# Performance work log

Measured on AMD Instinct MI355X. Metric: run time of the kernel, lower is better.

Reference implementation:

```python
import jax, jax.numpy as jnp
import numpy as np
import itertools

B, RES, RES_, STRIDE = 256, 14, 7, 2
N, N_ = RES * RES, RES_ * RES_
IN_DIM, OUT_DIM = 384, 512
H, KD, AR = 12, 32, 2
D = AR * KD            # 64, per-head value dim
DH = D * H             # 768
NH_KD = KD * H         # 384
KV_H = DH + NH_KD      # 1152
EPS = 1e-5


def _bias_idxs():
    # Replicates the relative-offset indexing from __init__.
    points = list(itertools.product(range(RES), range(RES)))
    points_ = list(itertools.product(range(RES_), range(RES_)))
    offsets, idxs = {}, []
    for p1 in points_:
        for p2 in points:
            off = (abs(p1[0] * STRIDE - p2[0]), abs(p1[1] * STRIDE - p2[1]))
            if off not in offsets:
                offsets[off] = len(offsets)
            idxs.append(offsets[off])
    return np.array(idxs, dtype=np.int32).reshape(N_, N), len(offsets)


def linear_bn(x, w, gamma, beta, mean, var):
    # Linear (no bias) followed by BatchNorm1d in inference form (fused affine).
    s = gamma / jnp.sqrt(var + EPS)
    return jnp.matmul(x, w.T) * s + (beta - mean * s)


def setup_inputs() -> dict:
    key = jax.random.key(0)
    ks = jax.random.split(key, 12)
    idxs_np, n_off = _bias_idxs()

    def bn_params(k, dim):
        k1, k2, k3, k4 = jax.random.split(k, 4)
        return (jax.random.normal(k1, (dim,)) * 0.1 + 1.0,   # gamma
                jax.random.normal(k2, (dim,)) * 0.1,          # beta
                jax.random.normal(k3, (dim,)) * 0.1,          # running_mean
                jax.random.uniform(k4, (dim,), minval=0.5, maxval=1.5))  # running_var

    kv_g, kv_b, kv_m, kv_v = bn_params(ks[1], KV_H)
    q_g, q_b, q_m, q_v = bn_params(ks[3], NH_KD)
    pr_g, pr_b, pr_m, pr_v = bn_params(ks[5], OUT_DIM)

    return {
        "x": jax.random.normal(ks[0], (B, N, IN_DIM), dtype=jnp.float32),
        "kv_w": jax.random.normal(ks[6], (KV_H, IN_DIM), dtype=jnp.float32) * (IN_DIM ** -0.5),
        "kv_g": kv_g, "kv_b": kv_b, "kv_m": kv_m, "kv_v": kv_v,
        "q_w": jax.random.normal(ks[7], (NH_KD, IN_DIM), dtype=jnp.float32) * (IN_DIM ** -0.5),
        "q_g": q_g, "q_b": q_b, "q_m": q_m, "q_v": q_v,
        "proj_w": jax.random.normal(ks[8], (OUT_DIM, DH), dtype=jnp.float32) * (DH ** -0.5),
        "proj_g": pr_g, "proj_b": pr_b, "proj_m": pr_m, "proj_v": pr_v,
        "attention_biases": jax.random.normal(ks[9], (H, n_off), dtype=jnp.float32) * 0.02,
        "bias_idxs": jnp.asarray(idxs_np),
    }


def reference(x, kv_w, kv_g, kv_b, kv_m, kv_v,
              q_w, q_g, q_b, q_m, q_v,
              proj_w, proj_g, proj_b, proj_m, proj_v,
              attention_biases, bias_idxs):
    Bsz = x.shape[0]
    scale = KD ** -0.5
    # kv projection: [B, N, H, KD+D] -> split into k, v
    kv = linear_bn(x, kv_w, kv_g, kv_b, kv_m, kv_v).reshape(Bsz, N, H, KD + D)
    k, v = kv[..., :KD], kv[..., KD:]
    # strided subsample of queries: [B, 14, 14, C] -> [B, 49, C]
    xs = x.reshape(Bsz, RES, RES, IN_DIM)[:, ::STRIDE, ::STRIDE].reshape(Bsz, N_, IN_DIM)
    q = linear_bn(xs, q_w, q_g, q_b, q_m, q_v).reshape(Bsz, N_, H, KD)
    # attention with gathered relative-position bias: bias [H, N_, N]
    bias = attention_biases[:, bias_idxs]
    attn = jnp.einsum('bqhd,bkhd->bhqk', q, k) * scale + bias
    attn = jax.nn.softmax(attn, axis=-1)
    out = jnp.einsum('bhqk,bkhd->bqhd', attn, v).reshape(Bsz, N_, DH)
    out = jax.nn.hard_swish(out)
    return linear_bn(out, proj_w, proj_g, proj_b, proj_m, proj_v)
```

## Files before the change

### kernel.cpp

```cpp
#include <hip/hip_runtime.h>
#include <hip/hip_bf16.h>
#include <math.h>

typedef unsigned short U16;
typedef unsigned int U32;
typedef __attribute__((ext_vector_type(8))) short bf8;
typedef __attribute__((ext_vector_type(4))) float f4;
typedef __attribute__((ext_vector_type(4))) unsigned short u16x4;

#define AS1 __attribute__((address_space(1)))
#define AS3 __attribute__((address_space(3)))

#define BSZ   256
#define NTOK  196
#define NQ    49
#define INDIM 384
#define OUTD  512
#define NH    12
#define DV    64
#define DHD   768
#define KVH   1152
#define NPADR 224

__device__ inline U16 f2bf(float f){
    __hip_bfloat16 h = __float2bfloat16(f);
    return *(U16*)&h;
}
__device__ inline f4 f4zero(){ f4 z; z[0]=0.f; z[1]=0.f; z[2]=0.f; z[3]=0.f; return z; }
__device__ inline bf8 bf8zero(){ bf8 v;
#pragma unroll
    for (int j=0;j<8;++j) v[j]=0; return v; }

#define XC_N   (BSZ*NTOK*INDIM/8)
#define XC_BLK (XC_N/256)
#define W1C (KVH*INDIM/8)
#define W2C (INDIM*INDIM/8)
#define W3C (OUTD*DHD/8)
#define WC_N   (W1C+W2C+W3C)
#define WC_BLK (WC_N/256)
#define BIAS_N   (NH*NQ*NTOK)
#define BIAS_BLK ((BIAS_N+255)/256)
#define BN_BLK   ((KVH+INDIM+OUTD)/256)
__global__ void k_prep(const float* __restrict__ x, U16* __restrict__ x_bf,
                       const float* __restrict__ w1, const float* __restrict__ w2,
                       const float* __restrict__ w3, U16* __restrict__ o1,
                       U16* __restrict__ o2, U16* __restrict__ o3,
                       const float* __restrict__ ab, const int* __restrict__ idxs, int n_off,
                       const float* __restrict__ g1, const float* __restrict__ b1,
                       const float* __restrict__ m1, const float* __restrict__ v1,
                       const float* __restrict__ g2, const float* __restrict__ b2,
                       const float* __restrict__ m2, const float* __restrict__ v2,
                       const float* __restrict__ g3, const float* __restrict__ b3,
                       const float* __restrict__ m3, const float* __restrict__ v3,
                       float* __restrict__ s1, float* __restrict__ bo1,
                       float* __restrict__ s2, float* __restrict__ bo2,
                       float* __restrict__ s3, float* __restrict__ bo3,
                       float* __restrict__ bias_out){
    const int blk = blockIdx.x;
    const int tid = threadIdx.x;
    if (blk < XC_BLK){
        int i = blk*256 + tid;
        const float* p = x + (size_t)i*8;
        U16 o[8];
#pragma unroll
        for (int j=0;j<8;++j) o[j] = f2bf(p[j]);
        *(bf8*)(x_bf + (size_t)i*8) = *(const bf8*)o;
    } else if (blk < XC_BLK + WC_BLK){
        int i = (blk-XC_BLK)*256 + tid;
        const float* p; U16* o;
        if (i < W1C){ p = w1 + (size_t)i*8; o = o1 + (size_t)i*8; }
        else if (i < W1C+W2C){ int k=i-W1C; p = w2 + (size_t)k*8; o = o2 + (size_t)k*8; }
        else { int k=i-W1C-W2C; p = w3 + (size_t)k*8; o = o3 + (size_t)k*8; }
        U16 t[8];
#pragma unroll
        for (int j=0;j<8;++j) t[j] = f2bf(p[j]);
        *(bf8*)o = *(const bf8*)t;
    } else if (blk < XC_BLK + WC_BLK + BIAS_BLK){
        int i = (blk-XC_BLK-WC_BLK)*256 + tid;
        if (i < BIAS_N){
            int h = i / (NQ*NTOK);
            int qk = i - h*(NQ*NTOK);
            bias_out[i] = ab[h*n_off + idxs[qk]];
        }
    } else {
        int i = (blk-XC_BLK-WC_BLK-BIAS_BLK)*256 + tid;
        const float *g,*b,*m,*v; float *so,*bo; int k;
        if (i < KVH){ g=g1;b=b1;m=m1;v=v1;so=s1;bo=bo1;k=i; }
        else if (i < KVH+INDIM){ g=g2;b=b2;m=m2;v=v2;so=s2;bo=bo2;k=i-KVH; }
        else { g=g3;b=b3;m=m3;v=v3;so=s3;bo=bo3;k=i-KVH-INDIM; }
        float s = g[k] / sqrtf(v[k] + 1e-5f);
        so[k] = s;
        bo[k] = b[k] - m[k]*s;
    }
}

#define KLO 12800
__global__ __launch_bounds__(256,2) void k_fused(
    const U16* __restrict__ xbf, const U16* __restrict__ kvw, const U16* __restrict__ qo_,
    const float* __restrict__ skv, const float* __restrict__ bkv,
    const float* __restrict__ biasf, U16* __restrict__ aout)
{
    __shared__ U16 smem[20480];
    const int hw = blockIdx.x;
    const int bh = (hw & 7)*384 + (hw >> 3);
    const int b = bh / NH, h = bh - b*NH;
    const int tid = threadIdx.x, lane = tid & 63, w = tid >> 6;
    const int wm = w & 1, wn = w >> 1;
    const int l15 = lane & 15, oct = lane >> 4;

    U16* Ab[2] = { smem + 0,     smem + 7168 };
    U16* Bb[2] = { smem + 14336, smem + 17408 };

    U32 aoff[4];
#pragma unroll
    for (int c=0;c<3;++c){
        int s = c*256 + tid;
        int ach = s / NPADR, ar = s - ach*NPADR;
        int row = (ar < NTOK) ? ar : (NTOK-1);
        aoff[c] = (U32)(b*NTOK + row)*INDIM + ach*8;
    }
    {
        int s = 768 + (tid & 127);
        int ach = s / NPADR, ar = s - ach*NPADR;
        int row = (ar < NTOK) ? ar : (NTOK-1);
        aoff[3] = (U32)(b*NTOK + row)*INDIM + ach*8;
    }
    U32 boff[2];
    {
        int s0 = tid;
        int bc0 = s0 / 96, br0 = s0 - bc0*96;
        boff[0] = (U32)(h*96 + br0)*INDIM + bc0*8;
        int s1 = 128 + (tid | 128);
        int bc1 = s1 / 96, br1 = s1 - bc1*96;
        boff[1] = (U32)(h*96 + br1)*INDIM + bc1*8;
    }

    f4 acc[7][3];
#pragma unroll
    for (int i=0;i<7;++i)
#pragma unroll
        for (int j=0;j<3;++j) acc[i][j] = f4zero();

#define STAGE(buf, kb) do{ \
    _Pragma("unroll") \
    for (int c=0;c<3;++c) \
        __builtin_amdgcn_global_load_lds((const AS1 U32*)(xbf + aoff[c] + (kb)), \
            (AS3 U32*)(Ab[buf] + (c*256+tid)*8), 16, 0, 0); \
    if (tid < 128) \
        __builtin_amdgcn_global_load_lds((const AS1 U32*)(xbf + aoff[3] + (kb)), \
            (AS3 U32*)(Ab[buf] + (768+tid)*8), 16, 0, 0); \
    __builtin_amdgcn_global_load_lds((const AS1 U32*)(kvw + boff[0] + (kb)), \
        (AS3 U32*)(Bb[buf] + tid*8), 16, 0, 0); \
    if (tid >= 128) \
        __builtin_amdgcn_global_load_lds((const AS1 U32*)(kvw + boff[1] + (kb)), \
            (AS3 U32*)(Bb[buf] + (128+tid)*8), 16, 0, 0); \
}while(0)

    STAGE(0, 0);
    asm volatile("s_waitcnt vmcnt(0)" ::: "memory");
    __builtin_amdgcn_sched_barrier(0);
    __builtin_amdgcn_s_barrier();
    __builtin_amdgcn_sched_barrier(0);

#pragma unroll
    for (int kt=0; kt<12; ++kt){
        const int cur = kt & 1;
        if (kt < 11) STAGE(cur^1, (kt+1)*32);
        __builtin_amdgcn_sched_barrier(0);
        bf8 af[7], bfr[3];
#pragma unroll
        for (int i=0;i<7;++i)
            af[i]  = *(const bf8*)(Ab[cur] + (oct*NPADR + wm*112 + i*16 + l15)*8);
#pragma unroll
        for (int j=0;j<3;++j)
            bfr[j] = *(const bf8*)(Bb[cur] + (oct*96 + wn*48 + j*16 + l15)*8);
        __builtin_amdgcn_s_setprio(1);
#pragma unroll
        for (int i=0;i<7;++i)
#pragma unroll
            for (int j=0;j<3;++j)
                acc[i][j] = __builtin_amdgcn_mfma_f32_16x16x32_bf16(af[i], bfr[j], acc[i][j], 0, 0, 0);
        __builtin_amdgcn_s_setprio(0);
        __builtin_amdgcn_sched_barrier(0);
        asm volatile("s_waitcnt vmcnt(0)" ::: "memory");
        __builtin_amdgcn_s_barrier();
        __builtin_amdgcn_sched_barrier(0);
    }
#undef STAGE

#pragma unroll
    for (int j=0;j<3;++j){
        const int cc = wn*48 + j*16 + l15;
        const float sc = skv[h*96 + cc];
        const float bi = bkv[h*96 + cc];
#pragma unroll
        for (int i=0;i<7;++i){
            const int n0 = wm*112 + i*16 + oct*4;
            if (cc < 32){
#pragma unroll
                for (int r=0;r<4;++r)
                    smem[KLO + ((cc>>3)*NPADR + n0 + r)*8 + (cc&7)] = f2bf(acc[i][j][r]*sc + bi);
            } else if (n0 < 200){
                const int dv = cc - 32;
                u16x4 pk;
#pragma unroll
                for (int r=0;r<4;++r) pk[r] = f2bf(acc[i][j][r]*sc + bi);
                *(u16x4*)(smem + ((n0>>3)*64 + dv)*8 + (oct&1)*4) = pk;
            }
        }
    }
    __syncthreads();

    const int qg = w*16 + l15;
    bf8 qf = bf8zero();
    if (qg < NQ) qf = *(const bf8*)(qo_ + ((size_t)(b*NQ + qg))*INDIM + h*32 + oct*8);

    f4 sacc[14];
#pragma unroll
    for (int mt=0;mt<14;++mt) sacc[mt] = f4zero();
#pragma unroll
    for (int mt=0;mt<14;++mt){
        const bf8 kf = *(const bf8*)(smem + KLO + (oct*NPADR + mt*16 + l15)*8);
        sacc[mt] = __builtin_amdgcn_mfma_f32_16x16x32_bf16(kf, qf, sacc[mt], 0, 0, 0);
    }

    const float scale = 0.17677669529663689f;
    float mx = -1e30f;
#pragma unroll
    for (int mt=0;mt<14;++mt){
        const int n0 = mt*16 + oct*4;
        f4 bi4 = f4zero();
        if (qg < NQ && n0 < NTOK) bi4 = *(const f4*)(biasf + ((size_t)h*NQ + qg)*NTOK + n0);
#pragma unroll
        for (int r=0;r<4;++r){
            float s = (n0 + r < NTOK) ? sacc[mt][r]*scale + bi4[r] : -1e30f;
            sacc[mt][r] = s;
            mx = fmaxf(mx, s);
        }
    }
    mx = fmaxf(mx, __shfl_xor(mx, 16));
    mx = fmaxf(mx, __shfl_xor(mx, 32));

    float sum = 0.f;
#pragma unroll
    for (int mt=0;mt<14;++mt){
#pragma unroll
        for (int r=0;r<4;++r){
            float p = (mt*16 + oct*4 + r < NTOK) ? __expf(sacc[mt][r] - mx) : 0.f;
            sacc[mt][r] = p;
            sum += p;
        }
    }
    sum += __shfl_xor(sum, 16);
    sum += __shfl_xor(sum, 32);
    const float inv = 1.f / sum;

    const int src1 = l15 + (oct & 1)*32;
    const int src2 = src1 + 16;
    const bool hiT = (oct >> 1) != 0;
    f4 pacc[4];
#pragma unroll
    for (int dt=0;dt<4;++dt) pacc[dt] = f4zero();
#pragma unroll
    for (int kt=0;kt<7;++kt){
        const int m0 = 2*kt, m1 = 2*kt+1;
        U32 q00 = (U32)f2bf(sacc[m0][0]*inv) | ((U32)f2bf(sacc[m0][1]*inv) << 16);
        U32 q01 = (U32)f2bf(sacc[m0][2]*inv) | ((U32)f2bf(sacc[m0][3]*inv) << 16);
        U32 q10 = (U32)f2bf(sacc[m1][0]*inv) | ((U32)f2bf(sacc[m1][1]*inv) << 16);
        U32 q11 = (U32)f2bf(sacc[m1][2]*inv) | ((U32)f2bf(sacc[m1][3]*inv) << 16);
        U32 a0 = __shfl(q00, src1), a1 = __shfl(q01, src1);
        U32 c0 = __shfl(q10, src1), c1 = __shfl(q11, src1);
        U32 b0 = __shfl(q00, src2), b1 = __shfl(q01, src2);
        U32 d0 = __shfl(q10, src2), d1 = __shfl(q11, src2);
        union { U32 u[4]; bf8 v; } pu;
        pu.u[0] = hiT ? c0 : a0;
        pu.u[1] = hiT ? c1 : a1;
        pu.u[2] = hiT ? d0 : b0;
        pu.u[3] = hiT ? d1 : b1;
#pragma unroll
        for (int dt=0;dt<4;++dt){
            const bf8 vf = *(const bf8*)(smem + ((kt*4 + oct)*64 + dt*16 + l15)*8);
            pacc[dt] = __builtin_amdgcn_mfma_f32_16x16x32_bf16(pu.v, vf, pacc[dt], 0, 0, 0);
        }
    }

#pragma unroll
    for (int dt=0;dt<4;++dt){
#pragma unroll
        for (int r=0;r<4;++r){
            const int qo2 = w*16 + oct*4 + r;
            if (qo2 < NQ){
                const int d = dt*16 + l15;
                float v = pacc[dt][r];
                float tt = fminf(fmaxf(v + 3.f, 0.f), 6.f);
                aout[((size_t)(b*NQ + qo2))*DHD + h*DV + d] = f2bf(v * tt * (1.f/6.f));
            }
        }
    }
}

template<int EPI, int NK, int KD, int NTILN, int NWG, bool SUB>
__global__ __launch_bounds__(256,2) void k_g64(
    const U16* __restrict__ A, const U16* __restrict__ Bw,
    const float* __restrict__ s_arr, const float* __restrict__ b_arr,
    U16* __restrict__ o16, float* __restrict__ o32)
{
    __shared__ U16 smem[24576];
    U16* Ab[2] = { smem,          smem + 8192 };
    U16* Bb[2] = { smem + 16384,  smem + 20480 };
    constexpr int QQ = NWG/8, RR = NWG%8;
    const int xcd = blockIdx.x & 7, rest = blockIdx.x >> 3;
    const int l = (xcd < RR ? xcd*(QQ+1) : RR*(QQ+1) + (xcd-RR)*QQ) + rest;
    const int mtl = l / NTILN, ntl = l - mtl*NTILN;
    const int gm0 = mtl*128, gn0 = ntl*64;
    const int tid  = threadIdx.x;
    const int lane = tid & 63;
    const int w    = tid >> 6;
    const int wm   = w & 1, wn = w >> 1;
    const int l15  = lane & 15, oct = lane >> 4;

    f4 acc[4][2];
#pragma unroll
    for (int i=0;i<4;++i)
#pragma unroll
        for (int j=0;j<2;++j) acc[i][j] = f4zero();

    U32 aoff[4], boff[2];
#pragma unroll
    for (int c=0;c<4;++c){
        int slot = c*256 + tid;
        int row = slot & 127, ch = slot >> 7;
        int grow = gm0 + row;
        if (SUB){
            int b2 = grow / NQ, qq = grow - b2*NQ;
            grow = b2*NTOK + 28*(qq/7) + 2*(qq%7);
        }
        aoff[c] = (U32)grow*KD + ch*8;
    }
#pragma unroll
    for (int c=0;c<2;++c){
        int slot = c*256 + tid;
        int row = slot & 63, ch = slot >> 6;
        boff[c] = (U32)(gn0 + row)*KD + ch*8;
    }

#define STG(buf, kb) do{ \
    _Pragma("unroll") \
    for (int c=0;c<4;++c) \
        __builtin_amdgcn_global_load_lds((const AS1 U32*)(A + aoff[c] + (kb)), \
            (AS3 U32*)(Ab[buf] + (c*256+tid)*8), 16, 0, 0); \
    _Pragma("unroll") \
    for (int c=0;c<2;++c) \
        __builtin_amdgcn_global_load_lds((const AS1 U32*)(Bw + boff[c] + (kb)), \
            (AS3 U32*)(Bb[buf] + (c*256+tid)*8), 16, 0, 0); \
}while(0)

    STG(0, 0);

#pragma unroll
    for (int kt=0; kt<NK; ++kt){
        const int cur = kt & 1;
        if (kt+1 < NK){
            STG(cur^1, (kt+1)*64);
            asm volatile("s_waitcnt vmcnt(6)" ::: "memory");
        } else {
            asm volatile("s_waitcnt vmcnt(0)" ::: "memory");
        }
        __builtin_amdgcn_sched_barrier(0);
        __builtin_amdgcn_s_barrier();
        __builtin_amdgcn_sched_barrier(0);

#pragma unroll
        for (int kk=0;kk<2;++kk){
            bf8 af[4], bfr[2];
#pragma unroll
            for (int i=0;i<4;++i)
                af[i]  = *(const bf8*)(Ab[cur] + ((kk*4+oct)*128 + wm*64 + i*16 + l15)*8);
#pragma unroll
            for (int j=0;j<2;++j)
                bfr[j] = *(const bf8*)(Bb[cur] + ((kk*4+oct)*64 + wn*32 + j*16 + l15)*8);
            __builtin_amdgcn_s_setprio(1);
#pragma unroll
            for (int i=0;i<4;++i)
#pragma unroll
                for (int j=0;j<2;++j)
                    acc[i][j] = __builtin_amdgcn_mfma_f32_16x16x32_bf16(af[i], bfr[j], acc[i][j], 0, 0, 0);
            __builtin_amdgcn_s_setprio(0);
        }
        __builtin_amdgcn_sched_barrier(0);
        __builtin_amdgcn_s_barrier();
        __builtin_amdgcn_sched_barrier(0);
    }
#undef STG

#pragma unroll
    for (int j=0;j<2;++j){
        const int col = gn0 + wn*32 + j*16 + l15;
        const float sc = s_arr[col];
        const float bi = b_arr[col];
#pragma unroll
        for (int i=0;i<4;++i){
            const int row0 = gm0 + wm*64 + i*16 + oct*4;
#pragma unroll
            for (int r=0;r<4;++r){
                const float val = acc[i][j][r]*sc + bi;
                if (EPI == 0) o16[(size_t)(row0+r)*INDIM + col] = f2bf(val);
                else          o32[(size_t)(row0+r)*OUTD  + col] = val;
            }
        }
    }
}

extern "C" void kernel_launch(void* const* d_in, const int* in_sizes, int n_in,
                              void* d_out, int out_size, void* d_ws, size_t ws_size,
                              hipStream_t stream)
{
    const float* x    = (const float*)d_in[0];
    const float* kv_w = (const float*)d_in[1];
    const float* kv_g = (const float*)d_in[2];
    const float* kv_b = (const float*)d_in[3];
    const float* kv_m = (const float*)d_in[4];
    const float* kv_v = (const float*)d_in[5];
    const float* q_w  = (const float*)d_in[6];
    const float* q_g  = (const float*)d_in[7];
    const float* q_b  = (const float*)d_in[8];
    const float* q_m  = (const float*)d_in[9];
    const float* q_v  = (const float*)d_in[10];
    const float* pr_w = (const float*)d_in[11];
    const float* pr_g = (const float*)d_in[12];
    const float* pr_b = (const float*)d_in[13];
    const float* pr_m = (const float*)d_in[14];
    const float* pr_v = (const float*)d_in[15];
    const float* ab   = (const float*)d_in[16];
    const int*  idxs  = (const int*)d_in[17];
    const int n_off = in_sizes[16] / NH;

    char* ws = (char*)d_ws;
    size_t off = 0;
    auto alloc = [&](size_t bytes)->char*{
        char* p = ws + off; off += (bytes + 255) & ~(size_t)255; return p;
    };
    U16*   x_bf   = (U16*)  alloc((size_t)BSZ*NTOK*INDIM*2);
    U16*   kvw_bf = (U16*)  alloc((size_t)KVH*INDIM*2);
    U16*   qw_bf  = (U16*)  alloc((size_t)INDIM*INDIM*2);
    U16*   prw_bf = (U16*)  alloc((size_t)OUTD*DHD*2);
    float* s_kv   = (float*)alloc(KVH*4);
    float* b_kv   = (float*)alloc(KVH*4);
    float* s_q    = (float*)alloc(INDIM*4);
    float* b_q    = (float*)alloc(INDIM*4);
    float* s_pr   = (float*)alloc(OUTD*4);
    float* b_pr   = (float*)alloc(OUTD*4);
    float* biasf  = (float*)alloc(((size_t)NH*NQ*NTOK + 256)*4);
    U16*   q_out  = (U16*)  alloc((size_t)BSZ*NQ*INDIM*2);
    U16*   a_out  = (U16*)  alloc((size_t)BSZ*NQ*DHD*2);
    if (off > ws_size) return;

    k_prep<<<XC_BLK + WC_BLK + BIAS_BLK + BN_BLK, 256, 0, stream>>>(
        x, x_bf, kv_w, q_w, pr_w, kvw_bf, qw_bf, prw_bf,
        ab, idxs, n_off,
        kv_g, kv_b, kv_m, kv_v, q_g, q_b, q_m, q_v, pr_g, pr_b, pr_m, pr_v,
        s_kv, b_kv, s_q, b_q, s_pr, b_pr, biasf);

    k_g64<0, 6, INDIM, 6, 588, true><<<588, 256, 0, stream>>>(
        x_bf, qw_bf, s_q, b_q, q_out, nullptr);
    k_fused<<<BSZ*NH, 256, 0, stream>>>(x_bf, kvw_bf, q_out, s_kv, b_kv, biasf, a_out);
    k_g64<1, 12, DHD, 8, 784, false><<<784, 256, 0, stream>>>(
        a_out, prw_bf, s_pr, b_pr, nullptr, (float*)d_out);
}
```

Before: 180.0 us.

## Fuse query projection into fused attention kernel by widening KV GEMM tile

Drops the separate Q-projection GEMM launch. The fused per-(batch,head) kernel now also multiplies x by the 32 query-weight rows for its head, widening the B tile from 96 to 128 columns. Only the even-row/even-column tokens are kept and written to shared memory as Q. This removes one kernel launch and the q_out round trip through global memory. In exchange every block computes Q for all 196 tokens rather than 49, about 33% more MFMA work in the projection loop, and shared memory use per block grows.

```diff
diff --git a/kernel.cpp b/kernel.cpp
--- a/kernel.cpp
+++ b/kernel.cpp
@@ -27,9 +27,6 @@
     return *(U16*)&h;
 }
 __device__ inline f4 f4zero(){ f4 z; z[0]=0.f; z[1]=0.f; z[2]=0.f; z[3]=0.f; return z; }
-__device__ inline bf8 bf8zero(){ bf8 v;
-#pragma unroll
-    for (int j=0;j<8;++j) v[j]=0; return v; }
 
 #define XC_N   (BSZ*NTOK*INDIM/8)
 #define XC_BLK (XC_N/256)
@@ -95,12 +92,14 @@
 }
 
 #define KLO 12800
+#define QLO 19968
 __global__ __launch_bounds__(256,2) void k_fused(
-    const U16* __restrict__ xbf, const U16* __restrict__ kvw, const U16* __restrict__ qo_,
+    const U16* __restrict__ xbf, const U16* __restrict__ kvw, const U16* __restrict__ qw,
     const float* __restrict__ skv, const float* __restrict__ bkv,
+    const float* __restrict__ sq,  const float* __restrict__ bq,
     const float* __restrict__ biasf, U16* __restrict__ aout)
 {
-    __shared__ U16 smem[20480];
+    __shared__ U16 smem[22528];
     const int hw = blockIdx.x;
     const int bh = (hw & 7)*384 + (hw >> 3);
     const int b = bh / NH, h = bh - b*NH;
@@ -109,7 +108,7 @@
     const int l15 = lane & 15, oct = lane >> 4;
 
     U16* Ab[2] = { smem + 0,     smem + 7168 };
-    U16* Bb[2] = { smem + 14336, smem + 17408 };
+    U16* Bb[2] = { smem + 14336, smem + 18432 };
 
     U32 aoff[4];
 #pragma unroll
@@ -125,21 +124,20 @@
         int row = (ar < NTOK) ? ar : (NTOK-1);
         aoff[3] = (U32)(b*NTOK + row)*INDIM + ach*8;
     }
-    U32 boff[2];
-    {
-        int s0 = tid;
-        int bc0 = s0 / 96, br0 = s0 - bc0*96;
-        boff[0] = (U32)(h*96 + br0)*INDIM + bc0*8;
-        int s1 = 128 + (tid | 128);
-        int bc1 = s1 / 96, br1 = s1 - bc1*96;
-        boff[1] = (U32)(h*96 + br1)*INDIM + bc1*8;
-    }
-
-    f4 acc[7][3];
+    const U16* bbase[2];
+#pragma unroll
+    for (int c=0;c<2;++c){
+        int s = c*256 + tid;
+        int bc = s >> 7, br = s & 127;
+        bbase[c] = (br < 96) ? kvw + ((size_t)(h*96 + br))*INDIM + bc*8
+                             : qw  + ((size_t)(h*32 + (br-96)))*INDIM + bc*8;
+    }
+
+    f4 acc[7][4];
 #pragma unroll
     for (int i=0;i<7;++i)
 #pragma unroll
-        for (int j=0;j<3;++j) acc[i][j] = f4zero();
+        for (int j=0;j<4;++j) acc[i][j] = f4zero();
 
 #define STAGE(buf, kb) do{ \
     _Pragma("unroll") \
@@ -149,11 +147,10 @@
     if (tid < 128) \
         __builtin_amdgcn_global_load_lds((const AS1 U32*)(xbf + aoff[3] + (kb)), \
             (AS3 U32*)(Ab[buf] + (768+tid)*8), 16, 0, 0); \
-    __builtin_amdgcn_global_load_lds((const AS1 U32*)(kvw + boff[0] + (kb)), \
-        (AS3 U32*)(Bb[buf] + tid*8), 16, 0, 0); \
-    if (tid >= 128) \
-        __builtin_amdgcn_global_load_lds((const AS1 U32*)(kvw + boff[1] + (kb)), \
-            (AS3 U32*)(Bb[buf] + (128+tid)*8), 16, 0, 0); \
+    _Pragma("unroll") \
+    for (int c=0;c<2;++c) \
+        __builtin_amdgcn_global_load_lds((const AS1 U32*)(bbase[c] + (kb)), \
+            (AS3 U32*)(Bb[buf] + (c*256+tid)*8), 16, 0, 0); \
 }while(0)
 
     STAGE(0, 0);
@@ -167,18 +164,18 @@
         const int cur = kt & 1;
         if (kt < 11) STAGE(cur^1, (kt+1)*32);
         __builtin_amdgcn_sched_barrier(0);
-        bf8 af[7], bfr[3];
+        bf8 af[7], bfr[4];
 #pragma unroll
         for (int i=0;i<7;++i)
             af[i]  = *(const bf8*)(Ab[cur] + (oct*NPADR + wm*112 + i*16 + l15)*8);
 #pragma unroll
-        for (int j=0;j<3;++j)
-            bfr[j] = *(const bf8*)(Bb[cur] + (oct*96 + wn*48 + j*16 + l15)*8);
+        for (int j=0;j<4;++j)
+            bfr[j] = *(const bf8*)(Bb[cur] + (oct*128 + wn*64 + j*16 + l15)*8);
         __builtin_amdgcn_s_setprio(1);
 #pragma unroll
         for (int i=0;i<7;++i)
 #pragma unroll
-            for (int j=0;j<3;++j)
+            for (int j=0;j<4;++j)
                 acc[i][j] = __builtin_amdgcn_mfma_f32_16x16x32_bf16(af[i], bfr[j], acc[i][j], 0, 0, 0);
         __builtin_amdgcn_s_setprio(0);
         __builtin_amdgcn_sched_barrier(0);
@@ -189,10 +186,11 @@
 #undef STAGE
 
 #pragma unroll
-    for (int j=0;j<3;++j){
-        const int cc = wn*48 + j*16 + l15;
-        const float sc = skv[h*96 + cc];
-        const float bi = bkv[h*96 + cc];
+    for (int j=0;j<4;++j){
+        const int cc = wn*64 + j*16 + l15;
+        float sc, bi;
+        if (cc < 96){ sc = skv[h*96 + cc]; bi = bkv[h*96 + cc]; }
+        else        { sc = sq[h*32 + (cc-96)]; bi = bq[h*32 + (cc-96)]; }
 #pragma unroll
         for (int i=0;i<7;++i){
             const int n0 = wm*112 + i*16 + oct*4;
@@ -200,20 +198,34 @@
 #pragma unroll
                 for (int r=0;r<4;++r)
                     smem[KLO + ((cc>>3)*NPADR + n0 + r)*8 + (cc&7)] = f2bf(acc[i][j][r]*sc + bi);
-            } else if (n0 < 200){
-                const int dv = cc - 32;
-                u16x4 pk;
-#pragma unroll
-                for (int r=0;r<4;++r) pk[r] = f2bf(acc[i][j][r]*sc + bi);
-                *(u16x4*)(smem + ((n0>>3)*64 + dv)*8 + (oct&1)*4) = pk;
+            } else if (cc < 96){
+                if (n0 < 200){
+                    const int dv = cc - 32;
+                    u16x4 pk;
+#pragma unroll
+                    for (int r=0;r<4;++r) pk[r] = f2bf(acc[i][j][r]*sc + bi);
+                    *(u16x4*)(smem + ((n0>>3)*64 + dv)*8 + (oct&1)*4) = pk;
+                }
+            } else {
+                const int dq = cc - 96;
+#pragma unroll
+                for (int r=0;r<4;++r){
+                    const int n = n0 + r;
+                    if (n < NTOK && (n & 1) == 0){
+                        const int dn = n / 28, nm = n - dn*28;
+                        if (nm < 14){
+                            const int qg2 = dn*7 + (nm >> 1);
+                            smem[QLO + ((dq>>3)*64 + qg2)*8 + (dq&7)] = f2bf(acc[i][j][r]*sc + bi);
+                        }
+                    }
+                }
             }
         }
     }
     __syncthreads();
 
     const int qg = w*16 + l15;
-    bf8 qf = bf8zero();
-    if (qg < NQ) qf = *(const bf8*)(qo_ + ((size_t)(b*NQ + qg))*INDIM + h*32 + oct*8);
+    const bf8 qf = *(const bf8*)(smem + QLO + (oct*64 + qg)*8);
 
     f4 sacc[14];
 #pragma unroll
@@ -299,19 +311,18 @@
     }
 }
 
-template<int EPI, int NK, int KD, int NTILN, int NWG, bool SUB>
-__global__ __launch_bounds__(256,2) void k_g64(
+__global__ __launch_bounds__(256,2) void k_proj(
     const U16* __restrict__ A, const U16* __restrict__ Bw,
     const float* __restrict__ s_arr, const float* __restrict__ b_arr,
-    U16* __restrict__ o16, float* __restrict__ o32)
+    float* __restrict__ o32)
 {
     __shared__ U16 smem[24576];
     U16* Ab[2] = { smem,          smem + 8192 };
     U16* Bb[2] = { smem + 16384,  smem + 20480 };
-    constexpr int QQ = NWG/8, RR = NWG%8;
+    constexpr int NWG = 784, QQ = NWG/8, RR = NWG%8;
     const int xcd = blockIdx.x & 7, rest = blockIdx.x >> 3;
     const int l = (xcd < RR ? xcd*(QQ+1) : RR*(QQ+1) + (xcd-RR)*QQ) + rest;
-    const int mtl = l / NTILN, ntl = l - mtl*NTILN;
+    const int mtl = l / 8, ntl = l - mtl*8;
     const int gm0 = mtl*128, gn0 = ntl*64;
     const int tid  = threadIdx.x;
     const int lane = tid & 63;
@@ -330,18 +341,13 @@
     for (int c=0;c<4;++c){
         int slot = c*256 + tid;
         int row = slot & 127, ch = slot >> 7;
-        int grow = gm0 + row;
-        if (SUB){
-            int b2 = grow / NQ, qq = grow - b2*NQ;
-            grow = b2*NTOK + 28*(qq/7) + 2*(qq%7);
-        }
-        aoff[c] = (U32)grow*KD + ch*8;
+        aoff[c] = (U32)(gm0 + row)*DHD + ch*8;
     }
 #pragma unroll
     for (int c=0;c<2;++c){
         int slot = c*256 + tid;
         int row = slot & 63, ch = slot >> 6;
-        boff[c] = (U32)(gn0 + row)*KD + ch*8;
+        boff[c] = (U32)(gn0 + row)*DHD + ch*8;
     }
 
 #define STG(buf, kb) do{ \
@@ -358,9 +364,9 @@
     STG(0, 0);
 
 #pragma unroll
-    for (int kt=0; kt<NK; ++kt){
+    for (int kt=0; kt<12; ++kt){
         const int cur = kt & 1;
-        if (kt+1 < NK){
+        if (kt+1 < 12){
             STG(cur^1, (kt+1)*64);
             asm volatile("s_waitcnt vmcnt(6)" ::: "memory");
         } else {
@@ -402,11 +408,8 @@
         for (int i=0;i<4;++i){
             const int row0 = gm0 + wm*64 + i*16 + oct*4;
 #pragma unroll
-            for (int r=0;r<4;++r){
-                const float val = acc[i][j][r]*sc + bi;
-                if (EPI == 0) o16[(size_t)(row0+r)*INDIM + col] = f2bf(val);
-                else          o32[(size_t)(row0+r)*OUTD  + col] = val;
-            }
+            for (int r=0;r<4;++r)
+                o32[(size_t)(row0+r)*OUTD + col] = acc[i][j][r]*sc + bi;
         }
     }
 }
@@ -451,7 +454,6 @@
     float* s_pr   = (float*)alloc(OUTD*4);
     float* b_pr   = (float*)alloc(OUTD*4);
     float* biasf  = (float*)alloc(((size_t)NH*NQ*NTOK + 256)*4);
-    U16*   q_out  = (U16*)  alloc((size_t)BSZ*NQ*INDIM*2);
     U16*   a_out  = (U16*)  alloc((size_t)BSZ*NQ*DHD*2);
     if (off > ws_size) return;
 
@@ -461,9 +463,7 @@
         kv_g, kv_b, kv_m, kv_v, q_g, q_b, q_m, q_v, pr_g, pr_b, pr_m, pr_v,
         s_kv, b_kv, s_q, b_q, s_pr, b_pr, biasf);
 
-    k_g64<0, 6, INDIM, 6, 588, true><<<588, 256, 0, stream>>>(
-        x_bf, qw_bf, s_q, b_q, q_out, nullptr);
-    k_fused<<<BSZ*NH, 256, 0, stream>>>(x_bf, kvw_bf, q_out, s_kv, b_kv, biasf, a_out);
-    k_g64<1, 12, DHD, 8, 784, false><<<784, 256, 0, stream>>>(
-        a_out, prw_bf, s_pr, b_pr, nullptr, (float*)d_out);
+    k_fused<<<BSZ*NH, 256, 0, stream>>>(x_bf, kvw_bf, qw_bf, s_kv, b_kv, s_q, b_q,
+                                        biasf, a_out);
+    k_proj<<<784, 256, 0, stream>>>(a_out, prw_bf, s_pr, b_pr, (float*)d_out);
 }
```

Measured after the change: 195.1 us. 1.08x slower.

## Process two heads per workgroup in fused attention kernel to share x tiles

Applied to the files above, without the earlier changes.

The fused kv-projection plus attention kernel now handles two heads per 512-thread workgroup instead of one head per 256-thread workgroup. The x tile staged in LDS is reused across both heads' kv weight columns, halving redundant x loads from global memory. It doubles LDS use per block and changes launch bounds to one block of 512 threads, which may reduce occupancy and latency hiding.

```diff
diff --git a/kernel.cpp b/kernel.cpp
--- a/kernel.cpp
+++ b/kernel.cpp
@@ -94,45 +94,44 @@
     }
 }
 
-#define KLO 12800
-__global__ __launch_bounds__(256,2) void k_fused(
+#define HSZ 19968
+#define KLR 12800
+__global__ __launch_bounds__(512,1) void k_fused(
     const U16* __restrict__ xbf, const U16* __restrict__ kvw, const U16* __restrict__ qo_,
     const float* __restrict__ skv, const float* __restrict__ bkv,
     const float* __restrict__ biasf, U16* __restrict__ aout)
 {
-    __shared__ U16 smem[20480];
+    __shared__ U16 smem[39936];
     const int hw = blockIdx.x;
-    const int bh = (hw & 7)*384 + (hw >> 3);
-    const int b = bh / NH, h = bh - b*NH;
+    const int ph = (hw & 7)*192 + (hw >> 3);
+    const int b = ph / 6, hp = ph - b*6;
     const int tid = threadIdx.x, lane = tid & 63, w = tid >> 6;
-    const int wm = w & 1, wn = w >> 1;
+    const int wm = w & 1, wc = w >> 1;
     const int l15 = lane & 15, oct = lane >> 4;
 
     U16* Ab[2] = { smem + 0,     smem + 7168 };
-    U16* Bb[2] = { smem + 14336, smem + 17408 };
-
-    U32 aoff[4];
-#pragma unroll
-    for (int c=0;c<3;++c){
-        int s = c*256 + tid;
+    U16* Bb[2] = { smem + 14336, smem + 20480 };
+
+    U32 aoff[2];
+    {
+        int s = tid;
         int ach = s / NPADR, ar = s - ach*NPADR;
         int row = (ar < NTOK) ? ar : (NTOK-1);
-        aoff[c] = (U32)(b*NTOK + row)*INDIM + ach*8;
-    }
-    {
-        int s = 768 + (tid & 127);
-        int ach = s / NPADR, ar = s - ach*NPADR;
-        int row = (ar < NTOK) ? ar : (NTOK-1);
-        aoff[3] = (U32)(b*NTOK + row)*INDIM + ach*8;
+        aoff[0] = (U32)(b*NTOK + row)*INDIM + ach*8;
+        s = 512 + tid;
+        ach = s / NPADR; ar = s - ach*NPADR;
+        row = (ar < NTOK) ? ar : (NTOK-1);
+        if (ach > 3) ach = 3;
+        aoff[1] = (U32)(b*NTOK + row)*INDIM + ach*8;
     }
     U32 boff[2];
     {
-        int s0 = tid;
-        int bc0 = s0 / 96, br0 = s0 - bc0*96;
-        boff[0] = (U32)(h*96 + br0)*INDIM + bc0*8;
-        int s1 = 128 + (tid | 128);
-        int bc1 = s1 / 96, br1 = s1 - bc1*96;
-        boff[1] = (U32)(h*96 + br1)*INDIM + bc1*8;
+        int s = tid;
+        int bch = s / 192, br = s - bch*192;
+        boff[0] = (U32)(hp*192 + br)*INDIM + bch*8;
+        s = 512 + (tid & 255);
+        bch = s / 192; br = s - bch*192;
+        boff[1] = (U32)(hp*192 + br)*INDIM + bch*8;
     }
 
     f4 acc[7][3];
@@ -142,18 +141,16 @@
         for (int j=0;j<3;++j) acc[i][j] = f4zero();
 
 #define STAGE(buf, kb) do{ \
-    _Pragma("unroll") \
-    for (int c=0;c<3;++c) \
-        __builtin_amdgcn_global_load_lds((const AS1 U32*)(xbf + aoff[c] + (kb)), \
-            (AS3 U32*)(Ab[buf] + (c*256+tid)*8), 16, 0, 0); \
-    if (tid < 128) \
-        __builtin_amdgcn_global_load_lds((const AS1 U32*)(xbf + aoff[3] + (kb)), \
-            (AS3 U32*)(Ab[buf] + (768+tid)*8), 16, 0, 0); \
+    __builtin_amdgcn_global_load_lds((const AS1 U32*)(xbf + aoff[0] + (kb)), \
+        (AS3 U32*)(Ab[buf] + tid*8), 16, 0, 0); \
+    if (tid < 384) \
+        __builtin_amdgcn_global_load_lds((const AS1 U32*)(xbf + aoff[1] + (kb)), \
+            (AS3 U32*)(Ab[buf] + (512+tid)*8), 16, 0, 0); \
     __builtin_amdgcn_global_load_lds((const AS1 U32*)(kvw + boff[0] + (kb)), \
         (AS3 U32*)(Bb[buf] + tid*8), 16, 0, 0); \
-    if (tid >= 128) \
+    if (tid < 256) \
         __builtin_amdgcn_global_load_lds((const AS1 U32*)(kvw + boff[1] + (kb)), \
-            (AS3 U32*)(Bb[buf] + (128+tid)*8), 16, 0, 0); \
+            (AS3 U32*)(Bb[buf] + (512+tid)*8), 16, 0, 0); \
 }while(0)
 
     STAGE(0, 0);
@@ -173,7 +170,7 @@
             af[i]  = *(const bf8*)(Ab[cur] + (oct*NPADR + wm*112 + i*16 + l15)*8);
 #pragma unroll
         for (int j=0;j<3;++j)
-            bfr[j] = *(const bf8*)(Bb[cur] + (oct*96 + wn*48 + j*16 + l15)*8);
+            bfr[j] = *(const bf8*)(Bb[cur] + (oct*192 + wc*48 + j*16 + l15)*8);
         __builtin_amdgcn_s_setprio(1);
 #pragma unroll
         for (int i=0;i<7;++i)
@@ -190,28 +187,36 @@
 
 #pragma unroll
     for (int j=0;j<3;++j){
-        const int cc = wn*48 + j*16 + l15;
-        const float sc = skv[h*96 + cc];
-        const float bi = bkv[h*96 + cc];
+        const int cc = wc*48 + j*16 + l15;
+        const int t = (cc >= 96) ? 1 : 0;
+        const int ccl = cc - t*96;
+        const int hh = hp*2 + t;
+        const float sc = skv[hh*96 + ccl];
+        const float bi = bkv[hh*96 + ccl];
+        const int base = t*HSZ;
 #pragma unroll
         for (int i=0;i<7;++i){
             const int n0 = wm*112 + i*16 + oct*4;
-            if (cc < 32){
+            if (ccl < 32){
 #pragma unroll
                 for (int r=0;r<4;++r)
-                    smem[KLO + ((cc>>3)*NPADR + n0 + r)*8 + (cc&7)] = f2bf(acc[i][j][r]*sc + bi);
+                    smem[base + KLR + ((ccl>>3)*NPADR + n0 + r)*8 + (ccl&7)] = f2bf(acc[i][j][r]*sc + bi);
             } else if (n0 < 200){
-                const int dv = cc - 32;
+                const int dv = ccl - 32;
                 u16x4 pk;
 #pragma unroll
                 for (int r=0;r<4;++r) pk[r] = f2bf(acc[i][j][r]*sc + bi);
-                *(u16x4*)(smem + ((n0>>3)*64 + dv)*8 + (oct&1)*4) = pk;
+                *(u16x4*)(smem + base + ((n0>>3)*64 + dv)*8 + (oct&1)*4) = pk;
             }
         }
     }
     __syncthreads();
 
-    const int qg = w*16 + l15;
+    const int t = w >> 2;
+    const int h = hp*2 + t;
+    const U16* VLa = smem + t*HSZ;
+    const U16* KLa = VLa + KLR;
+    const int qg = (w&3)*16 + l15;
     bf8 qf = bf8zero();
     if (qg < NQ) qf = *(const bf8*)(qo_ + ((size_t)(b*NQ + qg))*INDIM + h*32 + oct*8);
 
@@ -220,7 +225,7 @@
     for (int mt=0;mt<14;++mt) sacc[mt] = f4zero();
 #pragma unroll
     for (int mt=0;mt<14;++mt){
-        const bf8 kf = *(const bf8*)(smem + KLO + (oct*NPADR + mt*16 + l15)*8);
+        const bf8 kf = *(const bf8*)(KLa + (oct*NPADR + mt*16 + l15)*8);
         sacc[mt] = __builtin_amdgcn_mfma_f32_16x16x32_bf16(kf, qf, sacc[mt], 0, 0, 0);
     }
 
@@ -279,7 +284,7 @@
         pu.u[3] = hiT ? d1 : b1;
 #pragma unroll
         for (int dt=0;dt<4;++dt){
-            const bf8 vf = *(const bf8*)(smem + ((kt*4 + oct)*64 + dt*16 + l15)*8);
+            const bf8 vf = *(const bf8*)(VLa + ((kt*4 + oct)*64 + dt*16 + l15)*8);
             pacc[dt] = __builtin_amdgcn_mfma_f32_16x16x32_bf16(pu.v, vf, pacc[dt], 0, 0, 0);
         }
     }
@@ -288,7 +293,7 @@
     for (int dt=0;dt<4;++dt){
 #pragma unroll
         for (int r=0;r<4;++r){
-            const int qo2 = w*16 + oct*4 + r;
+            const int qo2 = (w&3)*16 + oct*4 + r;
             if (qo2 < NQ){
                 const int d = dt*16 + l15;
                 float v = pacc[dt][r];
@@ -463,7 +468,7 @@
 
     k_g64<0, 6, INDIM, 6, 588, true><<<588, 256, 0, stream>>>(
         x_bf, qw_bf, s_q, b_q, q_out, nullptr);
-    k_fused<<<BSZ*NH, 256, 0, stream>>>(x_bf, kvw_bf, q_out, s_kv, b_kv, biasf, a_out);
+    k_fused<<<BSZ*NH/2, 512, 0, stream>>>(x_bf, kvw_bf, q_out, s_kv, b_kv, biasf, a_out);
     k_g64<1, 12, DHD, 8, 784, false><<<784, 256, 0, stream>>>(
         a_out, prw_bf, s_pr, b_pr, nullptr, (float*)d_out);
 }
```

Result: slower. 185.6 us (+3.1%).
